# Performance work log

Hardware: AMD Instinct MI355X
Metric: run time of the kernel (lower is better)

The kernel has to match this reference:

```python
import jax, jax.numpy as jnp
from jax import lax
import numpy as np

EPS = 1e-5  # BatchNorm eps


def _gatv2(x, src, dst, Wl, Wr, att, bias, heads, d, concat):
    # x: [B, N, Fin]; src/dst: [E] (self-loops appended, PyG add_self_loops=True)
    B, N, _ = x.shape
    xl = jnp.einsum('bnf,of->bno', x, Wl).reshape(B, N, heads, d)  # source proj
    xr = jnp.einsum('bnf,of->bno', x, Wr).reshape(B, N, heads, d)  # target proj
    e = jax.nn.leaky_relu(xl[:, src] + xr[:, dst], 0.2)            # [B,E,H,d]
    logit = jnp.einsum('behd,hd->beh', e, att)                     # [B,E,H]
    seg_max = jax.vmap(lambda v: jax.ops.segment_max(v, dst, num_segments=N))
    seg_sum = jax.vmap(lambda v: jax.ops.segment_sum(v, dst, num_segments=N))
    m = seg_max(logit)                                             # [B,N,H]
    p = jnp.exp(logit - m[:, dst])
    alpha = p / seg_sum(p)[:, dst]                                 # edge softmax over targets
    out = seg_sum(alpha[..., None] * xl[:, src])                   # [B,N,H,d]
    out = out.reshape(B, N, heads * d) if concat else out.mean(2)
    return out + bias


def _bn(h, g, b, m, v):  # BatchNorm1d, eval mode (running stats)
    return (h - m) * (g / jnp.sqrt(v + EPS)) + b


def _lstm_layer(seq, Wih, Whh, bih, bhh):
    # seq: [BN, T, Hin]; gate order i,f,g,o (PyTorch)
    BN, T, _ = seq.shape
    H = Whh.shape[1]
    pre = jnp.einsum('bti,gi->tbg', seq, Wih) + bih + bhh          # [T,BN,4H]
    def step(carry, xp):
        h, c = carry
        g = xp + h @ Whh.T
        i, f, gg, o = jnp.split(g, 4, axis=-1)
        c = jax.nn.sigmoid(f) * c + jax.nn.sigmoid(i) * jnp.tanh(gg)
        h = jax.nn.sigmoid(o) * jnp.tanh(c)
        return (h, c), h
    h0 = jnp.zeros((BN, H), seq.dtype)
    _, hs = lax.scan(step, (h0, h0), pre)
    return jnp.swapaxes(hs, 0, 1)                                  # [BN,T,H]


def forward(x, edge_index, Wp, bp, Wl1, Wr1, a1, bg1, g1, be1, m1, v1,
            Wl2, Wr2, a2, bg2, g2, be2, m2, v2,
            Wih0, Whh0, bih0, bhh0, Wih1, Whh1, bih1, bhh1,
            Wa, ba, Ws1, bs1, Ws2, bs2, Wh1, bh1, Wh2, bh2):
    b, t, n, f = x.shape
    H = Wp.shape[0]
    loops = jnp.arange(n, dtype=edge_index.dtype)
    src = jnp.concatenate([edge_index[0], loops])
    dst = jnp.concatenate([edge_index[1], loops])
    xt = x.reshape(b * t, n, f)  # batch all (b,t) graph passes together
    h1 = jax.nn.elu(_bn(_gatv2(xt, src, dst, Wl1, Wr1, a1, bg1, 2, H, True), g1, be1, m1, v1))
    # dropout is identity in eval mode
    h2 = jax.nn.elu(_bn(_gatv2(h1, src, dst, Wl2, Wr2, a2, bg2, 1, H, False), g2, be2, m2, v2))
    h = h2 + jnp.einsum('bnf,hf->bnh', xt, Wp) + bp                # residual input_proj
    sp = h.reshape(b * n, t, H)  # replicates torch .view(b*n,t,H) on contiguous [b,t,n,H]
    lo = _lstm_layer(_lstm_layer(sp, Wih0, Whh0, bih0, bhh0), Wih1, Whh1, bih1, bhh1)
    aw = jax.nn.softmax(jnp.einsum('bth,oh->bto', lo, Wa) + ba, axis=1)
    ctx = (aw * lo).sum(1)                                         # [b*n, H]
    nb = Ws1.shape[1]
    sk = x[:, -1, :, :nb].reshape(b * n, nb)
    sk = jax.nn.gelu(sk @ Ws1.T + bs1, approximate=False) @ Ws2.T + bs2
    z = jnp.concatenate([ctx, sk], axis=1)
    z = jax.nn.gelu(z @ Wh1.T + bh1, approximate=False) @ Wh2.T + bh2
    return z.reshape(b, n, 1)


def setup_inputs() -> dict:
    key = jax.random.key(0)
    ks = jax.random.split(key, 40)
    b, t, n, f, H, E, nb = 4, 16, 1000, 32, 128, 16000, 13
    p = lambda k, s: (jax.random.normal(k, s) * 0.05).astype(jnp.float32)
    x = jax.random.normal(ks[0], (b, t, n, f), jnp.float32)
    src = jax.random.randint(ks[1], (E,), 0, n)
    dst = (src + jax.random.randint(ks[2], (E,), 1, n)) % n  # no accidental self-loops
    edge_index = jnp.stack([src, dst]).astype(jnp.int32)
    return dict(
        x=x, edge_index=edge_index,
        Wp=p(ks[3], (H, f)), bp=p(ks[4], (H,)),
        Wl1=p(ks[5], (2 * H, f)), Wr1=p(ks[6], (2 * H, f)), a1=p(ks[7], (2, H)), bg1=p(ks[8], (2 * H,)),
        g1=1.0 + p(ks[9], (2 * H,)), be1=p(ks[10], (2 * H,)), m1=p(ks[11], (2 * H,)),
        v1=jax.random.uniform(ks[12], (2 * H,), minval=0.5, maxval=1.5),
        Wl2=p(ks[13], (H, 2 * H)), Wr2=p(ks[14], (H, 2 * H)), a2=p(ks[15], (1, H)), bg2=p(ks[16], (H,)),
        g2=1.0 + p(ks[17], (H,)), be2=p(ks[18], (H,)), m2=p(ks[19], (H,)),
        v2=jax.random.uniform(ks[20], (H,), minval=0.5, maxval=1.5),
        Wih0=p(ks[21], (4 * H, H)), Whh0=p(ks[22], (4 * H, H)), bih0=p(ks[23], (4 * H,)), bhh0=p(ks[24], (4 * H,)),
        Wih1=p(ks[25], (4 * H, H)), Whh1=p(ks[26], (4 * H, H)), bih1=p(ks[27], (4 * H,)), bhh1=p(ks[28], (4 * H,)),
        Wa=p(ks[29], (1, H)), ba=p(ks[30], (1,)),
        Ws1=p(ks[31], (H // 2, nb)), bs1=p(ks[32], (H // 2,)),
        Ws2=p(ks[33], (H // 4, H // 2)), bs2=p(ks[34], (H // 4,)),
        Wh1=p(ks[35], (H // 2, H + H // 4)), bh1=p(ks[36], (H // 2,)),
        Wh2=p(ks[37], (1, H // 2)), bh2=p(ks[38], (1,)))


def reference(x, edge_index, Wp, bp, Wl1, Wr1, a1, bg1, g1, be1, m1, v1,
              Wl2, Wr2, a2, bg2, g2, be2, m2, v2,
              Wih0, Whh0, bih0, bhh0, Wih1, Whh1, bih1, bhh1,
              Wa, ba, Ws1, bs1, Ws2, bs2, Wh1, bh1, Wh2, bh2):
    return forward(x, edge_index, Wp, bp, Wl1, Wr1, a1, bg1, g1, be1, m1, v1,
                   Wl2, Wr2, a2, bg2, g2, be2, m2, v2,
                   Wih0, Whh0, bih0, bhh0, Wih1, Whh1, bih1, bhh1,
                   Wa, ba, Ws1, bs1, Ws2, bs2, Wh1, bh1, Wh2, bh2)
```

## Files before the change

kernel.cpp:

```cpp
#include <hip/hip_runtime.h>
#include <hip/hip_fp16.h>

#define EPS_BN 1e-5f

typedef __attribute__((ext_vector_type(8))) short bf16x8;
typedef __attribute__((ext_vector_type(4))) float f32x4;

#define O_SRCD   0u
#define O_DSTD   17024u
#define O_COUNTS 34048u
#define O_OFFS   35072u
#define O_CURS   36096u
#define O_EIDX   37120u
#define O_PW1    54144u
#define O_PW2    74624u
#define O_LW     140160u
#define O_BCOMB  402304u
#define O_ABF    403328u
#define O_HWT    404352u
#define O_BIG0   417536u
#define O_BIG1   (O_BIG0 + 16384000u)
#define O_BIG2   (O_BIG1 + 16384000u)
#define O_BIG3   (O_BIG2 + 16384000u)
#define O_BIG4   (O_BIG3 + 8192000u)
#define O_SXL    (O_BIG4 + 8192000u)

__device__ __forceinline__ float rsum32(float p) {
  p += __shfl_xor(p, 1);  p += __shfl_xor(p, 2);  p += __shfl_xor(p, 4);
  p += __shfl_xor(p, 8);  p += __shfl_xor(p, 16); return p;
}
__device__ __forceinline__ float rsum64(float p) {
  p = rsum32(p); p += __shfl_xor(p, 32); return p;
}
__device__ __forceinline__ float eluf(float x)  { return x > 0.f ? x : expm1f(x); }
__device__ __forceinline__ float geluf(float x) { return 0.5f * x * (1.f + erff(x * 0.70710678118654752f)); }
__device__ __forceinline__ unsigned short f2bf(float f) {
  unsigned int u = __float_as_uint(f);
  u += 0x7FFFu + ((u >> 16) & 1u);
  return (unsigned short)(u >> 16);
}
__device__ __forceinline__ float bf2f(unsigned short h) {
  return __uint_as_float(((unsigned int)h) << 16);
}
__device__ __forceinline__ unsigned short f2h(float x) {
  __half h = __float2half(x);
  return *reinterpret_cast<unsigned short*>(&h);
}
__device__ __forceinline__ float h2f(unsigned short u) {
  __half h = *reinterpret_cast<__half*>(&u);
  return __half2float(h);
}
__device__ __forceinline__ void unpk(unsigned int w, float& lo, float& hi) {
  lo = __uint_as_float(w << 16);
  hi = __uint_as_float(w & 0xFFFF0000u);
}

__global__ __launch_bounds__(1024)
void prep_all(const int* __restrict__ ei, int* __restrict__ srcD,
              int* __restrict__ dstD, int* __restrict__ offs,
              int* __restrict__ esrc)
{
  __shared__ int cnt[1024];
  __shared__ int cur[1000];
  const int tid = threadIdx.x;
  cnt[tid] = 0;
  __syncthreads();
  for (int i = tid; i < 17000; i += 1024) {
    int s = (i < 16000) ? ei[i] : (i - 16000);
    int d = (i < 16000) ? ei[16000 + i] : (i - 16000);
    srcD[i] = s; dstD[i] = d;
    atomicAdd(&cnt[d], 1);
  }
  __syncthreads();
  int v = cnt[tid];
  for (int d = 1; d < 1024; d <<= 1) {
    int t = (tid >= d) ? cnt[tid - d] : 0;
    __syncthreads();
    cnt[tid] += t;
    __syncthreads();
  }
  if (tid < 1000) { offs[tid + 1] = cnt[tid]; cur[tid] = cnt[tid] - v; }
  if (tid == 0) offs[0] = 0;
  __syncthreads();
  for (int i = tid; i < 17000; i += 1024) {
    int p = atomicAdd(&cur[dstD[i]], 1);
    esrc[p] = srcD[i];
  }
}

__global__ void pack_kernel(
    const float* __restrict__ Wl1, const float* __restrict__ Wr1, const float* __restrict__ Wp,
    const float* __restrict__ Wl2, const float* __restrict__ Wr2,
    const float* __restrict__ Wih0, const float* __restrict__ Whh0,
    const float* __restrict__ bih0, const float* __restrict__ bhh0,
    const float* __restrict__ Wih1, const float* __restrict__ Whh1,
    const float* __restrict__ bih1, const float* __restrict__ bhh1,
    const float* __restrict__ g1, const float* __restrict__ be1, const float* __restrict__ m1,
    const float* __restrict__ v1, const float* __restrict__ bg1,
    const float* __restrict__ g2, const float* __restrict__ be2, const float* __restrict__ m2,
    const float* __restrict__ v2, const float* __restrict__ bg2,
    const float* __restrict__ Ws1, const float* __restrict__ Ws2, const float* __restrict__ Wh1,
    const float* __restrict__ a1, const float* __restrict__ a2,
    float* __restrict__ PW1, unsigned short* __restrict__ PW2Bu,
    unsigned short* __restrict__ PHHBu, unsigned short* __restrict__ PWBu,
    float* __restrict__ BC, float* __restrict__ ABF, float* __restrict__ HWT,
    float* __restrict__ C1F, float* __restrict__ C2F)
{
  int i = blockIdx.x * 256 + threadIdx.x;
  if (i < 262144) {
    int e = i & 7, lane = (i >> 3) & 63, gt = (i >> 9) & 31,
        kc = (i >> 14) & 3, sp = (i >> 16) & 1, L = (i >> 17) & 1;
    int gp = (gt << 4) + (lane & 15);
    int jj = gp >> 2, gate = gp & 3;
    int kk = (kc << 5) + ((lane >> 4) << 3) + e;
    const float* Wih = L ? Wih1 : Wih0;
    const float* Whh = L ? Whh1 : Whh0;
    float wv = Wih[(gate * 128 + jj) * 128 + kk];
    unsigned short hi = f2bf(wv);
    PWBu[i] = (sp == 0) ? hi : f2bf(wv - bf2f(hi));
    float hv = Whh[(gate * 128 + jj) * 128 + kk];
    unsigned short hhi = f2bf(hv);
    PHHBu[i] = (sp == 0) ? hhi : f2bf(hv - bf2f(hhi));
  }
  if (i < 131072) {
    int e = i & 7, lane = (i >> 3) & 63, ct = (i >> 9) & 15,
        kc = (i >> 13) & 7, sp = (i >> 16) & 1;
    int c = (ct << 4) + (lane & 15);
    int k = (kc << 5) + ((lane >> 4) << 3) + e;
    float wv2 = (c < 128) ? Wl2[c * 256 + k] : Wr2[(c - 128) * 256 + k];
    unsigned short hi = f2bf(wv2);
    PW2Bu[i] = (sp == 0) ? hi : f2bf(wv2 - bf2f(hi));
  }
  if (i < 20480) { int g = i % 640, k = i / 640;
    PW1[i] = (g < 256) ? Wl1[g * 32 + k] : (g < 512) ? Wr1[(g - 256) * 32 + k]
                                                     : Wp[(g - 512) * 32 + k]; }
  if (i < 1024) { int u = i & 3, jj = (i >> 2) & 127, L = i >> 9;
    BC[i] = (L ? bih1 : bih0)[u * 128 + jj] + (L ? bhh1 : bhh0)[u * 128 + jj]; }
  if (i < 768) {
    if (i < 256) ABF[i] = g1[i] * rsqrtf(v1[i] + EPS_BN);
    else if (i < 512) { int c = i - 256; float a = g1[c] * rsqrtf(v1[c] + EPS_BN);
      ABF[i] = (bg1[c] - m1[c]) * a + be1[c]; }
    else if (i < 640) { int c = i - 512; ABF[i] = g2[c] * rsqrtf(v2[c] + EPS_BN); }
    else { int c = i - 640; float a = g2[c] * rsqrtf(v2[c] + EPS_BN);
      ABF[i] = (bg2[c] - m2[c]) * a + be2[c]; }
  }
  if (i < 13120) {
    if (i < 832) { int l = i & 63, c = i >> 6; HWT[i] = Ws1[l * 13 + c]; }
    else if (i < 2880) { int k = i - 832; int l = k & 31, jj = k >> 5; HWT[i] = Ws2[l * 64 + jj]; }
    else { int k = i - 2880; int l = k & 63, r = k >> 6; HWT[i] = Wh1[l * 160 + r]; }
  }
  if (i < 64) {
    int k = i & 31, h = i >> 5;
    float s = 0.f;
    for (int j = 0; j < 128; ++j)
      s = fmaf(a1[h * 128 + j], Wl1[(h * 128 + j) * 32 + k], s);
    C1F[i] = 0.6f * s;
  }
  if (i < 256) {
    float s = 0.f;
    for (int c = 0; c < 128; ++c)
      s = fmaf(a2[c], Wl2[c * 256 + i], s);
    C2F[i] = 0.6f * s;
  }
}

__global__ __launch_bounds__(320)
void proj1_kernel(const float* __restrict__ X, const float* __restrict__ PW1,
                  const float* __restrict__ bp, const float* __restrict__ C1F,
                  unsigned short* __restrict__ XL1u,
                  float* __restrict__ XR1, float* __restrict__ XP,
                  float* __restrict__ SXL1)
{
  __shared__ __align__(16) float xs[32][16];
  const int tid = threadIdx.x;
  const int r0 = blockIdx.x * 16;
  for (int el = tid; el < 512; el += 320) {
    int r = el >> 5, k = el & 31;
    xs[k][r] = X[(size_t)(r0 + r) * 32 + k];
  }
  __syncthreads();
  if (tid < 32) {
    int r = tid & 15, h = tid >> 4;
    const float* c1 = C1F + h * 32;
    float s = 0.f;
    for (int k = 0; k < 32; ++k) s = fmaf(c1[k], xs[k][r], s);
    SXL1[(size_t)(r0 + r) * 2 + h] = s;
  }
  const int gA = tid, gB = tid + 320;
  float accA[16], accB[16];
  const float iB = (gB >= 512) ? bp[gB - 512] : 0.f;
  #pragma unroll
  for (int r = 0; r < 16; ++r) { accA[r] = 0.f; accB[r] = iB; }
  for (int k = 0; k < 32; ++k) {
    float wA = PW1[k * 640 + gA], wB = PW1[k * 640 + gB];
    float xv[16];
    #pragma unroll
    for (int q = 0; q < 4; ++q)
      *reinterpret_cast<float4*>(&xv[q * 4]) = *reinterpret_cast<const float4*>(&xs[k][q * 4]);
    #pragma unroll
    for (int r = 0; r < 16; ++r) {
      accA[r] = fmaf(wA, xv[r], accA[r]);
      accB[r] = fmaf(wB, xv[r], accB[r]);
    }
  }
  for (int r = 0; r < 16; ++r) {
    size_t row = r0 + r;
    if (gA < 256) XL1u[row * 256 + gA] = f2bf(accA[r]);
    else          XR1[row * 256 + (gA - 256)] = accA[r];
    if (gB < 512) XR1[row * 256 + (gB - 256)] = accB[r];
    else          XP[row * 128 + (gB - 512)] = accB[r];
  }
}

__global__ __launch_bounds__(256)
void gat1_kernel(const unsigned short* __restrict__ XLu, const float* __restrict__ XR,
                 const float* __restrict__ SXL,
                 const int* __restrict__ esrc, const int* __restrict__ offs,
                 const float* __restrict__ a1, const float* __restrict__ ABF,
                 const float* __restrict__ C2F,
                 float* __restrict__ H1, float* __restrict__ SXL2)
{
  const int lane = threadIdx.x & 63;
  const int wv = threadIdx.x >> 6;
  const int n = blockIdx.x * 4 + wv;
  const int b = blockIdx.y;
  const int epar = lane >> 5;
  const int head = (lane >> 4) & 1;
  const int li = lane & 15;
  const int f0 = head * 128 + li * 8;
  const int beg = offs[n];
  const int deg = offs[n + 1] - beg;
  const uint4* XLb = reinterpret_cast<const uint4*>(XLu) + (size_t)b * 32000 + (f0 >> 3);
  const float* SXLb = SXL + (size_t)b * 2000;
  float xr[8], av[8];
  {
    const float* xrp = XR + (size_t)(b * 1000 + n) * 256 + f0;
    float4 t0 = *reinterpret_cast<const float4*>(xrp);
    float4 t1 = *reinterpret_cast<const float4*>(xrp + 4);
    xr[0]=t0.x; xr[1]=t0.y; xr[2]=t0.z; xr[3]=t0.w;
    xr[4]=t1.x; xr[5]=t1.y; xr[6]=t1.z; xr[7]=t1.w;
    const float* ap = a1 + f0;
    float4 a0 = *reinterpret_cast<const float4*>(ap);
    float4 a1v = *reinterpret_cast<const float4*>(ap + 4);
    av[0]=a0.x; av[1]=a0.y; av[2]=a0.z; av[3]=a0.w;
    av[4]=a1v.x; av[5]=a1v.y; av[6]=a1v.z; av[7]=a1v.w;
  }
  float ssum = 0.f, acc[8];
  #pragma unroll
  for (int k = 0; k < 8; ++k) acc[k] = 0.f;
  bool v = epar < deg;
  int sC = esrc[beg + (v ? epar : 0)];
  uint4 u = XLb[(size_t)sC * 32];
  float slxC = SXLb[sC * 2 + head];
  for (int i0 = 0; i0 < deg; i0 += 2) {
    int nmy = i0 + 2 + epar;
    bool nv = nmy < deg;
    int sN = esrc[beg + (nv ? nmy : 0)];
    uint4 un = XLb[(size_t)sN * 32];
    float slxN = SXLb[sN * 2 + head];
    float x[8];
    unpk(u.x, x[0], x[1]); unpk(u.y, x[2], x[3]);
    unpk(u.z, x[4], x[5]); unpk(u.w, x[6], x[7]);
    float p = 0.f;
    #pragma unroll
    for (int k = 0; k < 8; ++k)
      p = fmaf(av[k], fabsf(x[k] + xr[k]), p);
    p += __shfl_xor(p, 1); p += __shfl_xor(p, 2);
    p += __shfl_xor(p, 4); p += __shfl_xor(p, 8);
    float we = v ? __expf(fmaf(0.4f, p, slxC)) : 0.f;
    ssum += we;
    #pragma unroll
    for (int k = 0; k < 8; ++k) acc[k] = fmaf(we, x[k], acc[k]);
    v = nv; u = un; slxC = slxN;
  }
  ssum += __shfl_xor(ssum, 32);
  float inv = 1.f / ssum;
  float A4[8], B4[8];
  {
    const float* aap = ABF + f0;
    float4 t0 = *reinterpret_cast<const float4*>(aap);
    float4 t1 = *reinterpret_cast<const float4*>(aap + 4);
    A4[0]=t0.x; A4[1]=t0.y; A4[2]=t0.z; A4[3]=t0.w;
    A4[4]=t1.x; A4[5]=t1.y; A4[6]=t1.z; A4[7]=t1.w;
    const float* bbp = ABF + 256 + f0;
    float4 s0v = *reinterpret_cast<const float4*>(bbp);
    float4 s1v = *reinterpret_cast<const float4*>(bbp + 4);
    B4[0]=s0v.x; B4[1]=s0v.y; B4[2]=s0v.z; B4[3]=s0v.w;
    B4[4]=s1v.x; B4[5]=s1v.y; B4[6]=s1v.z; B4[7]=s1v.w;
  }
  float o[8];
  #pragma unroll
  for (int k = 0; k < 8; ++k) {
    float A = acc[k] + __shfl_xor(acc[k], 32);
    o[k] = eluf(fmaf(A * inv, A4[k], B4[k]));
  }
  {
    const float* cp = C2F + f0;
    float4 c0 = *reinterpret_cast<const float4*>(cp);
    float4 c1 = *reinterpret_cast<const float4*>(cp + 4);
    float cc[8] = {c0.x, c0.y, c0.z, c0.w, c1.x, c1.y, c1.z, c1.w};
    float s2 = 0.f;
    #pragma unroll
    for (int k = 0; k < 8; ++k) s2 = fmaf(cc[k], o[k], s2);
    s2 += __shfl_xor(s2, 1); s2 += __shfl_xor(s2, 2);
    s2 += __shfl_xor(s2, 4); s2 += __shfl_xor(s2, 8);
    s2 += __shfl_xor(s2, 16);
    if (lane == 0) SXL2[(size_t)b * 1000 + n] = s2;
  }
  if (lane < 32) {
    float* hp = H1 + (size_t)(b * 1000 + n) * 256 + f0;
    *reinterpret_cast<float4*>(hp) = make_float4(o[0], o[1], o[2], o[3]);
    *reinterpret_cast<float4*>(hp + 4) = make_float4(o[4], o[5], o[6], o[7]);
  }
}

__global__ __launch_bounds__(512)
void proj2_kernel(const float* __restrict__ H1, const unsigned short* __restrict__ PW2B,
                  unsigned short* __restrict__ XL2u, float* __restrict__ XR2)
{
  const int tid = threadIdx.x;
  const int lane = tid & 63;
  const int wv = tid >> 6;
  const int l15 = lane & 15;
  const int kg = lane >> 4;
  const int r0 = blockIdx.x * 32;
  f32x4 acc[2][2];
  #pragma unroll
  for (int rt = 0; rt < 2; ++rt)
    #pragma unroll
    for (int ct = 0; ct < 2; ++ct)
      #pragma unroll
      for (int e = 0; e < 4; ++e) acc[rt][ct][e] = 0.f;
  for (int kc = 0; kc < 8; ++kc) {
    bf16x8 xh[2], xl[2];
    #pragma unroll
    for (int rt = 0; rt < 2; ++rt) {
      const float* xp = H1 + (size_t)(r0 + rt * 16 + l15) * 256 + (kc << 5) + (kg << 3);
      float4 va = *reinterpret_cast<const float4*>(xp);
      float4 vb = *reinterpret_cast<const float4*>(xp + 4);
      float xs[8] = {va.x, va.y, va.z, va.w, vb.x, vb.y, vb.z, vb.w};
      #pragma unroll
      for (int e = 0; e < 8; ++e) {
        unsigned short h = f2bf(xs[e]);
        xh[rt][e] = (short)h;
        xl[rt][e] = (short)f2bf(xs[e] - bf2f(h));
      }
    }
    #pragma unroll
    for (int ct = 0; ct < 2; ++ct) {
      const int ctg = (wv << 1) + ct;
      const unsigned short* wp = PW2B + ((size_t)(kc * 16 + ctg)) * 512 + lane * 8;
      bf16x8 whi = *reinterpret_cast<const bf16x8*>(wp);
      bf16x8 wlo = *reinterpret_cast<const bf16x8*>(wp + 65536);
      #pragma unroll
      for (int rt = 0; rt < 2; ++rt) {
        acc[rt][ct] = __builtin_amdgcn_mfma_f32_16x16x32_bf16(xh[rt], whi, acc[rt][ct], 0, 0, 0);
        acc[rt][ct] = __builtin_amdgcn_mfma_f32_16x16x32_bf16(xh[rt], wlo, acc[rt][ct], 0, 0, 0);
        acc[rt][ct] = __builtin_amdgcn_mfma_f32_16x16x32_bf16(xl[rt], whi, acc[rt][ct], 0, 0, 0);
      }
    }
  }
  #pragma unroll
  for (int ct = 0; ct < 2; ++ct) {
    const int col = (wv << 5) + (ct << 4) + l15;
    #pragma unroll
    for (int rt = 0; rt < 2; ++rt) {
      #pragma unroll
      for (int reg = 0; reg < 4; ++reg) {
        const int row = r0 + rt * 16 + (kg << 2) + reg;
        float val = acc[rt][ct][reg];
        if (col < 128) XL2u[(size_t)row * 128 + col] = f2bf(val);
        else           XR2[(size_t)row * 128 + (col - 128)] = val;
      }
    }
  }
}

__global__ __launch_bounds__(256)
void gat2_kernel(const unsigned short* __restrict__ XLu, const float* __restrict__ XR,
                 const float* __restrict__ SXL,
                 const int* __restrict__ esrc, const int* __restrict__ offs,
                 const float* __restrict__ a2, const float* __restrict__ ABF,
                 const float* __restrict__ XP, float* __restrict__ Hout)
{
  const int lane = threadIdx.x & 63;
  const int wv = threadIdx.x >> 6;
  const int n = blockIdx.x * 4 + wv;
  const int b = blockIdx.y;
  const int grp = lane >> 4;
  const int li = lane & 15;
  const int f0 = li * 8;
  const int beg = offs[n];
  const int deg = offs[n + 1] - beg;
  const uint4* XLb = reinterpret_cast<const uint4*>(XLu) + (size_t)b * 16000 + li;
  const float* SXLb = SXL + (size_t)b * 1000;
  float xr[8], av[8];
  {
    const float* xrp = XR + (size_t)(b * 1000 + n) * 128 + f0;
    float4 t0 = *reinterpret_cast<const float4*>(xrp);
    float4 t1 = *reinterpret_cast<const float4*>(xrp + 4);
    xr[0]=t0.x; xr[1]=t0.y; xr[2]=t0.z; xr[3]=t0.w;
    xr[4]=t1.x; xr[5]=t1.y; xr[6]=t1.z; xr[7]=t1.w;
    const float* ap = a2 + f0;
    float4 a0 = *reinterpret_cast<const float4*>(ap);
    float4 a1v = *reinterpret_cast<const float4*>(ap + 4);
    av[0]=a0.x; av[1]=a0.y; av[2]=a0.z; av[3]=a0.w;
    av[4]=a1v.x; av[5]=a1v.y; av[6]=a1v.z; av[7]=a1v.w;
  }
  float ssum = 0.f, acc[8];
  #pragma unroll
  for (int k = 0; k < 8; ++k) acc[k] = 0.f;
  bool v = grp < deg;
  int sC = esrc[beg + (v ? grp : 0)];
  uint4 u = XLb[(size_t)sC * 16];
  float slxC = SXLb[sC];
  for (int i0 = 0; i0 < deg; i0 += 4) {
    int nmy = i0 + 4 + grp;
    bool nv = nmy < deg;
    int sN = esrc[beg + (nv ? nmy : 0)];
    uint4 un = XLb[(size_t)sN * 16];
    float slxN = SXLb[sN];
    float x[8];
    unpk(u.x, x[0], x[1]); unpk(u.y, x[2], x[3]);
    unpk(u.z, x[4], x[5]); unpk(u.w, x[6], x[7]);
    float p = 0.f;
    #pragma unroll
    for (int k = 0; k < 8; ++k)
      p = fmaf(av[k], fabsf(x[k] + xr[k]), p);
    p += __shfl_xor(p, 1); p += __shfl_xor(p, 2);
    p += __shfl_xor(p, 4); p += __shfl_xor(p, 8);
    float we = v ? __expf(fmaf(0.4f, p, slxC)) : 0.f;
    ssum += we;
    #pragma unroll
    for (int k = 0; k < 8; ++k) acc[k] = fmaf(we, x[k], acc[k]);
    v = nv; u = un; slxC = slxN;
  }
  ssum += __shfl_xor(ssum, 16);
  ssum += __shfl_xor(ssum, 32);
  #pragma unroll
  for (int k = 0; k < 8; ++k) {
    acc[k] += __shfl_xor(acc[k], 16);
    acc[k] += __shfl_xor(acc[k], 32);
  }
  float inv = 1.f / ssum;
  if (lane < 16) {
    const float* aap = ABF + 512 + f0;
    float4 t0 = *reinterpret_cast<const float4*>(aap);
    float4 t1 = *reinterpret_cast<const float4*>(aap + 4);
    const float* bbp = ABF + 640 + f0;
    float4 s0v = *reinterpret_cast<const float4*>(bbp);
    float4 s1v = *reinterpret_cast<const float4*>(bbp + 4);
    const float* xpp = XP + (size_t)(b * 1000 + n) * 128 + f0;
    float4 p0 = *reinterpret_cast<const float4*>(xpp);
    float4 p1 = *reinterpret_cast<const float4*>(xpp + 4);
    float A4[8] = {t0.x, t0.y, t0.z, t0.w, t1.x, t1.y, t1.z, t1.w};
    float B4[8] = {s0v.x, s0v.y, s0v.z, s0v.w, s1v.x, s1v.y, s1v.z, s1v.w};
    float P4[8] = {p0.x, p0.y, p0.z, p0.w, p1.x, p1.y, p1.z, p1.w};
    float o[8];
    #pragma unroll
    for (int k = 0; k < 8; ++k)
      o[k] = eluf(fmaf(acc[k] * inv, A4[k], B4[k])) + P4[k];
    float* hp = Hout + (size_t)(b * 1000 + n) * 128 + f0;
    *reinterpret_cast<float4*>(hp) = make_float4(o[0], o[1], o[2], o[3]);
    *reinterpret_cast<float4*>(hp + 4) = make_float4(o[4], o[5], o[6], o[7]);
  }
}

__global__ __launch_bounds__(512)
void gemm_pre_kernel(const float* __restrict__ X, const unsigned short* __restrict__ PWB,
                     const float* __restrict__ BCL, unsigned short* __restrict__ PREh)
{
  const int tid = threadIdx.x;
  const int lane = tid & 63;
  const int wv = tid >> 6;
  const int l15 = lane & 15;
  const int kg = lane >> 4;
  const int r0 = blockIdx.x * 32;
  f32x4 acc[2][4];
  #pragma unroll
  for (int rt = 0; rt < 2; ++rt)
    #pragma unroll
    for (int gt = 0; gt < 4; ++gt)
      #pragma unroll
      for (int e = 0; e < 4; ++e) acc[rt][gt][e] = 0.f;
  for (int kc = 0; kc < 4; ++kc) {
    bf16x8 xh[2], xl[2];
    #pragma unroll
    for (int rt = 0; rt < 2; ++rt) {
      const float* xp = X + (size_t)(r0 + rt * 16 + l15) * 128 + (kc << 5) + (kg << 3);
      float4 va = *reinterpret_cast<const float4*>(xp);
      float4 vb = *reinterpret_cast<const float4*>(xp + 4);
      float xs[8] = {va.x, va.y, va.z, va.w, vb.x, vb.y, vb.z, vb.w};
      #pragma unroll
      for (int e = 0; e < 8; ++e) {
        unsigned short h = f2bf(xs[e]);
        xh[rt][e] = (short)h;
        xl[rt][e] = (short)f2bf(xs[e] - bf2f(h));
      }
    }
    #pragma unroll
    for (int gt = 0; gt < 4; ++gt) {
      const int gtg = (wv << 2) + gt;
      const unsigned short* wp = PWB + ((size_t)(kc * 32 + gtg)) * 512 + lane * 8;
      bf16x8 whi = *reinterpret_cast<const bf16x8*>(wp);
      bf16x8 wlo = *reinterpret_cast<const bf16x8*>(wp + 65536);
      #pragma unroll
      for (int rt = 0; rt < 2; ++rt) {
        acc[rt][gt] = __builtin_amdgcn_mfma_f32_16x16x32_bf16(xh[rt], whi, acc[rt][gt], 0, 0, 0);
        acc[rt][gt] = __builtin_amdgcn_mfma_f32_16x16x32_bf16(xh[rt], wlo, acc[rt][gt], 0, 0, 0);
        acc[rt][gt] = __builtin_amdgcn_mfma_f32_16x16x32_bf16(xl[rt], whi, acc[rt][gt], 0, 0, 0);
      }
    }
  }
  #pragma unroll
  for (int gt = 0; gt < 4; ++gt) {
    const int col = (wv << 6) + (gt << 4) + l15;
    const float bias = BCL[col];
    #pragma unroll
    for (int rt = 0; rt < 2; ++rt) {
      #pragma unroll
      for (int reg = 0; reg < 4; ++reg) {
        const int row = r0 + rt * 16 + (kg << 2) + reg;
        PREh[(size_t)row * 512 + col] = f2h(acc[rt][gt][reg] + bias);
      }
    }
  }
}

__device__ __forceinline__ float cellf(float4 g, float& c) {
  const float ig = 1.f / (1.f + __expf(-g.x));
  const float fg = 1.f / (1.f + __expf(-g.y));
  const float gg = tanhf(g.z);
  const float og = 1.f / (1.f + __expf(-g.w));
  c = fmaf(fg, c, ig * gg);
  return og * tanhf(c);
}

__global__ __launch_bounds__(512)
void rec2_kernel(const unsigned short* __restrict__ PREh,
                 const unsigned short* __restrict__ PHHB,
                 float* __restrict__ HOUT)
{
  __shared__ unsigned short whi[65536];
  __shared__ unsigned short afr[2][4][64][8];
  const int tid = threadIdx.x;
  const int lane = tid & 63;
  const int w = tid >> 6;
  const int l15 = lane & 15;
  const int kg = lane >> 4;
  const int q0 = blockIdx.x << 4;
  for (int i = tid; i < 8192; i += 512)
    reinterpret_cast<uint4*>(whi)[i] = reinterpret_cast<const uint4*>(PHHB)[i];
  reinterpret_cast<uint4*>(&afr[0][0][0][0])[tid] = make_uint4(0u, 0u, 0u, 0u);
  const unsigned short* wloG = PHHB + 65536;
  float cs[4] = {0.f, 0.f, 0.f, 0.f};
  const int qq = l15 & 3;
  const int uu = l15 >> 2;
  const int seq = (kg << 2) + qq;
  for (int t = 0; t < 16; ++t) {
    __syncthreads();
    bf16x8 ah[4], al[4];
    #pragma unroll
    for (int kc = 0; kc < 4; ++kc) {
      ah[kc] = *reinterpret_cast<const bf16x8*>(&afr[0][kc][lane][0]);
      al[kc] = *reinterpret_cast<const bf16x8*>(&afr[1][kc][lane][0]);
    }
    f32x4 acc[4];
    #pragma unroll
    for (int gl = 0; gl < 4; ++gl)
      #pragma unroll
      for (int e = 0; e < 4; ++e) acc[gl][e] = 0.f;
    #pragma unroll
    for (int gl = 0; gl < 4; ++gl) {
      const int gt = (w << 2) + gl;
      #pragma unroll
      for (int kc = 0; kc < 4; ++kc) {
        const int off = ((kc * 32 + gt) * 64 + lane) * 8;
        bf16x8 wh = *reinterpret_cast<const bf16x8*>(&whi[off]);
        bf16x8 wl = *reinterpret_cast<const bf16x8*>(&wloG[off]);
        acc[gl] = __builtin_amdgcn_mfma_f32_16x16x32_bf16(ah[kc], wh, acc[gl], 0, 0, 0);
        acc[gl] = __builtin_amdgcn_mfma_f32_16x16x32_bf16(ah[kc], wl, acc[gl], 0, 0, 0);
        acc[gl] = __builtin_amdgcn_mfma_f32_16x16x32_bf16(al[kc], wh, acc[gl], 0, 0, 0);
      }
    }
    __syncthreads();
    const int row = ((q0 + seq) << 4) + t;
    #pragma unroll
    for (int gl = 0; gl < 4; ++gl) {
      const int gt = (w << 2) + gl;
      float in0 = acc[gl][0], in1 = acc[gl][1], in2 = acc[gl][2], in3 = acc[gl][3];
      float s0 = __shfl_xor(in1, 1), s1 = __shfl_xor(in0, 1),
            s2 = __shfl_xor(in3, 1), s3 = __shfl_xor(in2, 1);
      const bool b0 = (qq & 1);
      float t0 = b0 ? s0 : in0;
      float t1 = b0 ? in1 : s1;
      float t2 = b0 ? s2 : in2;
      float t3 = b0 ? in3 : s3;
      float u0 = __shfl_xor(t2, 2), u1 = __shfl_xor(t3, 2),
            u2 = __shfl_xor(t0, 2), u3 = __shfl_xor(t1, 2);
      const bool b1 = (qq & 2);
      float g0 = b1 ? u0 : t0;
      float g1 = b1 ? u1 : t1;
      float g2 = b1 ? t2 : u2;
      float g3 = b1 ? t3 : u3;
      const unsigned short* pp = PREh + (size_t)row * 512 + (gt << 4) + (uu << 2);
      ushort4 pu = *reinterpret_cast<const ushort4*>(pp);
      float4 gv = make_float4(g0 + h2f(pu.x), g1 + h2f(pu.y),
                              g2 + h2f(pu.z), g3 + h2f(pu.w));
      float h = cellf(gv, cs[gl]);
      const int unit = (gt << 2) + uu;
      HOUT[(size_t)row * 128 + unit] = h;
      if (t < 15) {
        unsigned short hh = f2bf(h);
        unsigned short hl = f2bf(h - bf2f(hh));
        const int kc2 = unit >> 5;
        const int lane2 = seq | (((unit & 31) >> 3) << 4);
        const int e2 = unit & 7;
        afr[0][kc2][lane2][e2] = hh;
        afr[1][kc2][lane2][e2] = hl;
      }
    }
  }
}

__global__ __launch_bounds__(64)
void attn_kernel(const float* __restrict__ LO, const float* __restrict__ X,
                 const float* __restrict__ Wa, const float* __restrict__ ba,
                 const float* __restrict__ bs1, const float* __restrict__ bs2,
                 const float* __restrict__ bh1, const float* __restrict__ bh2,
                 const float* __restrict__ Wh2, const float* __restrict__ HWT,
                 float* __restrict__ out)
{
  const int q = blockIdx.x, l = threadIdx.x;
  const float* lob = LO + (size_t)q * 2048;
  float loa[16], lobv[16];
  #pragma unroll
  for (int t = 0; t < 16; ++t) {
    loa[t]  = lob[t * 128 + l];
    lobv[t] = lob[t * 128 + 64 + l];
  }
  const float wa = Wa[l], wb = Wa[64 + l];
  float sc[16];
  #pragma unroll
  for (int t = 0; t < 16; ++t) sc[t] = rsum64(loa[t] * wa + lobv[t] * wb) + ba[0];
  float mx = sc[0];
  #pragma unroll
  for (int t = 1; t < 16; ++t) mx = fmaxf(mx, sc[t]);
  float den = 0.f;
  #pragma unroll
  for (int t = 0; t < 16; ++t) { sc[t] = __expf(sc[t] - mx); den += sc[t]; }
  const float inv = 1.f / den;
  float ca = 0.f, cb = 0.f;
  #pragma unroll
  for (int t = 0; t < 16; ++t) {
    float wgt = sc[t] * inv;
    ca = fmaf(wgt, loa[t], ca);
    cb = fmaf(wgt, lobv[t], cb);
  }
  __shared__ float zsh[160];
  __shared__ float hsk[64];
  __shared__ float skin[16];
  zsh[l] = ca; zsh[64 + l] = cb;
  const int bb = q / 1000, nn = q - bb * 1000;
  if (l < 13) skin[l] = X[(size_t)((bb * 16 + 15) * 1000 + nn) * 32 + l];
  __syncthreads();
  float h1 = bs1[l];
  for (int c = 0; c < 13; ++c) h1 = fmaf(skin[c], HWT[c * 64 + l], h1);
  h1 = geluf(h1);
  hsk[l] = h1;
  __syncthreads();
  if (l < 32) {
    float a = bs2[l];
    for (int jj = 0; jj < 64; ++jj) a = fmaf(hsk[jj], HWT[832 + jj * 32 + l], a);
    zsh[128 + l] = a;
  }
  __syncthreads();
  float hh = bh1[l];
  for (int r = 0; r < 160; ++r) hh = fmaf(zsh[r], HWT[2880 + r * 64 + l], hh);
  hh = geluf(hh);
  float s = rsum64(hh * Wh2[l]);
  if (l == 0) out[q] = s + bh2[0];
}

extern "C" void kernel_launch(void* const* d_in, const int* in_sizes, int n_in,
                              void* d_out, int out_size, void* d_ws, size_t ws_size,
                              hipStream_t stream)
{
  const float* x    = (const float*)d_in[0];
  const int*   ei   = (const int*)d_in[1];
  const float* Wp   = (const float*)d_in[2];
  const float* bp   = (const float*)d_in[3];
  const float* Wl1  = (const float*)d_in[4];
  const float* Wr1  = (const float*)d_in[5];
  const float* a1   = (const float*)d_in[6];
  const float* bg1  = (const float*)d_in[7];
  const float* g1   = (const float*)d_in[8];
  const float* be1  = (const float*)d_in[9];
  const float* m1   = (const float*)d_in[10];
  const float* v1   = (const float*)d_in[11];
  const float* Wl2  = (const float*)d_in[12];
  const float* Wr2  = (const float*)d_in[13];
  const float* a2   = (const float*)d_in[14];
  const float* bg2  = (const float*)d_in[15];
  const float* g2   = (const float*)d_in[16];
  const float* be2  = (const float*)d_in[17];
  const float* m2   = (const float*)d_in[18];
  const float* v2   = (const float*)d_in[19];
  const float* Wih0 = (const float*)d_in[20];
  const float* Whh0 = (const float*)d_in[21];
  const float* bih0 = (const float*)d_in[22];
  const float* bhh0 = (const float*)d_in[23];
  const float* Wih1 = (const float*)d_in[24];
  const float* Whh1 = (const float*)d_in[25];
  const float* bih1 = (const float*)d_in[26];
  const float* bhh1 = (const float*)d_in[27];
  const float* Wa   = (const float*)d_in[28];
  const float* ba   = (const float*)d_in[29];
  const float* Ws1  = (const float*)d_in[30];
  const float* bs1  = (const float*)d_in[31];
  const float* Ws2  = (const float*)d_in[32];
  const float* bs2  = (const float*)d_in[33];
  const float* Wh1  = (const float*)d_in[34];
  const float* bh1  = (const float*)d_in[35];
  const float* Wh2  = (const float*)d_in[36];
  const float* bh2  = (const float*)d_in[37];

  float* ws = (float*)d_ws;
  int* srcD   = (int*)(ws + O_SRCD);
  int* dstD   = (int*)(ws + O_DSTD);
  int* offs   = (int*)(ws + O_OFFS);
  int* esrc   = (int*)(ws + O_EIDX);
  float* PW1  = ws + O_PW1;
  unsigned short* PW2Bu = (unsigned short*)(ws + O_PW2);
  unsigned short* PHHBu = (unsigned short*)(ws + O_LW);
  unsigned short* PWBu  = (unsigned short*)(ws + O_LW + 131072u);
  float* BC   = ws + O_BCOMB;
  float* ABF  = ws + O_ABF;
  float* HWT  = ws + O_HWT;
  unsigned short* XL1u = (unsigned short*)(ws + O_BIG0);
  float* XR1  = ws + O_BIG1;
  float* H1   = ws + O_BIG2;
  float* XP   = ws + O_BIG3;
  float* Hres = ws + O_BIG4;
  unsigned short* XL2u = (unsigned short*)(ws + O_BIG0);
  float* XR2  = ws + O_BIG0 + 8192000u;
  unsigned short* PREh = (unsigned short*)(ws + O_BIG0);
  float* H1SEQ = ws + O_BIG2;
  float* LOp  = ws + O_BIG3;
  float* SXL1 = ws + O_SXL;
  float* SXL2 = ws + O_SXL + 128000u;
  float* C1F  = ws + O_SXL + 192000u;
  float* C2F  = ws + O_SXL + 192064u;
  float* outp = (float*)d_out;

  prep_all<<<1, 1024, 0, stream>>>(ei, srcD, dstD, offs, esrc);
  pack_kernel<<<1024, 256, 0, stream>>>(Wl1, Wr1, Wp, Wl2, Wr2,
      Wih0, Whh0, bih0, bhh0, Wih1, Whh1, bih1, bhh1,
      g1, be1, m1, v1, bg1, g2, be2, m2, v2, bg2,
      Ws1, Ws2, Wh1, a1, a2, PW1, PW2Bu, PHHBu, PWBu, BC, ABF, HWT, C1F, C2F);
  proj1_kernel<<<4000, 320, 0, stream>>>(x, PW1, bp, C1F, XL1u, XR1, XP, SXL1);
  gat1_kernel<<<dim3(250, 64), 256, 0, stream>>>(XL1u, XR1, SXL1, esrc, offs, a1, ABF,
                                                 C2F, H1, SXL2);
  proj2_kernel<<<2000, 512, 0, stream>>>(H1, PW2Bu, XL2u, XR2);
  gat2_kernel<<<dim3(250, 64), 256, 0, stream>>>(XL2u, XR2, SXL2, esrc, offs, a2, ABF, XP, Hres);
  gemm_pre_kernel<<<2000, 512, 0, stream>>>(Hres, PWBu, BC, PREh);
  rec2_kernel<<<250, 512, 0, stream>>>(PREh, PHHBu, H1SEQ);
  gemm_pre_kernel<<<2000, 512, 0, stream>>>(H1SEQ, PWBu + 131072u, BC + 512, PREh);
  rec2_kernel<<<250, 512, 0, stream>>>(PREh, PHHBu + 131072u, LOp);
  attn_kernel<<<4000, 64, 0, stream>>>(LOp, x, Wa, ba, bs1, bs2, bh1, bh2, Wh2, HWT, outp);
}
```

Before: 560.0 us.

## Store intermediate activations as bf16 and drop split-precision MFMA passes

All large intermediate tensors (XR1, XP, H1, XR2, Hres, LSTM hidden outputs) are now written and read as bf16 instead of fp32, roughly halving global memory traffic between kernels. The GEMMs for proj2 and the LSTM input projection now load bf16 activations directly and skip the hi/lo activation split, going from three MFMAs per tile to two. The single-block edge CSR build is also split into four multi-block kernels. The cost is lower precision in the activations passed between stages and three extra kernel launches.

Result: faster. 477.9 us (-14.7%).

```diff
diff --git a/kernel.cpp b/kernel.cpp
--- a/kernel.cpp
+++ b/kernel.cpp
@@ -54,38 +54,45 @@
   lo = __uint_as_float(w << 16);
   hi = __uint_as_float(w & 0xFFFF0000u);
 }
-
-__global__ __launch_bounds__(1024)
-void prep_all(const int* __restrict__ ei, int* __restrict__ srcD,
-              int* __restrict__ dstD, int* __restrict__ offs,
-              int* __restrict__ esrc)
-{
-  __shared__ int cnt[1024];
-  __shared__ int cur[1000];
-  const int tid = threadIdx.x;
-  cnt[tid] = 0;
-  __syncthreads();
-  for (int i = tid; i < 17000; i += 1024) {
+__device__ __forceinline__ void unpk8(uint4 u, float (&x)[8]) {
+  unpk(u.x, x[0], x[1]); unpk(u.y, x[2], x[3]);
+  unpk(u.z, x[4], x[5]); unpk(u.w, x[6], x[7]);
+}
+
+__global__ void prep_edges(const int* __restrict__ ei, int* __restrict__ srcD,
+                           int* __restrict__ dstD, int* __restrict__ counts) {
+  int i = blockIdx.x * 256 + threadIdx.x;
+  if (i < 1024) counts[i] = 0;
+  if (i < 17000) {
     int s = (i < 16000) ? ei[i] : (i - 16000);
     int d = (i < 16000) ? ei[16000 + i] : (i - 16000);
     srcD[i] = s; dstD[i] = d;
-    atomicAdd(&cnt[d], 1);
-  }
+  }
+}
+__global__ void hist_kernel(const int* __restrict__ dstD, int* __restrict__ counts) {
+  int i = blockIdx.x * 256 + threadIdx.x;
+  if (i < 17000) atomicAdd(&counts[dstD[i]], 1);
+}
+__global__ void scan_kernel(const int* __restrict__ counts, int* __restrict__ offs,
+                            int* __restrict__ curs) {
+  __shared__ int sh[1024];
+  int i = threadIdx.x;
+  int v = (i < 1000) ? counts[i] : 0;
+  sh[i] = v;
   __syncthreads();
-  int v = cnt[tid];
   for (int d = 1; d < 1024; d <<= 1) {
-    int t = (tid >= d) ? cnt[tid - d] : 0;
+    int t = (i >= d) ? sh[i - d] : 0;
     __syncthreads();
-    cnt[tid] += t;
+    sh[i] += t;
     __syncthreads();
   }
-  if (tid < 1000) { offs[tid + 1] = cnt[tid]; cur[tid] = cnt[tid] - v; }
-  if (tid == 0) offs[0] = 0;
-  __syncthreads();
-  for (int i = tid; i < 17000; i += 1024) {
-    int p = atomicAdd(&cur[dstD[i]], 1);
-    esrc[p] = srcD[i];
-  }
+  if (i < 1000) { offs[i + 1] = sh[i]; curs[i] = sh[i] - v; }
+  if (i == 0) offs[0] = 0;
+}
+__global__ void fill_kernel(const int* __restrict__ srcD, const int* __restrict__ dstD,
+                            int* __restrict__ curs, int* __restrict__ esrc) {
+  int i = blockIdx.x * 256 + threadIdx.x;
+  if (i < 17000) { int p = atomicAdd(&curs[dstD[i]], 1); esrc[p] = srcD[i]; }
 }
 
 __global__ void pack_kernel(
@@ -168,7 +175,7 @@
 void proj1_kernel(const float* __restrict__ X, const float* __restrict__ PW1,
                   const float* __restrict__ bp, const float* __restrict__ C1F,
                   unsigned short* __restrict__ XL1u,
-                  float* __restrict__ XR1, float* __restrict__ XP,
+                  unsigned short* __restrict__ XR1u, unsigned short* __restrict__ XPu,
                   float* __restrict__ SXL1)
 {
   __shared__ __align__(16) float xs[32][16];
@@ -206,19 +213,19 @@
   for (int r = 0; r < 16; ++r) {
     size_t row = r0 + r;
     if (gA < 256) XL1u[row * 256 + gA] = f2bf(accA[r]);
-    else          XR1[row * 256 + (gA - 256)] = accA[r];
-    if (gB < 512) XR1[row * 256 + (gB - 256)] = accB[r];
-    else          XP[row * 128 + (gB - 512)] = accB[r];
+    else          XR1u[row * 256 + (gA - 256)] = f2bf(accA[r]);
+    if (gB < 512) XR1u[row * 256 + (gB - 256)] = f2bf(accB[r]);
+    else          XPu[row * 128 + (gB - 512)] = f2bf(accB[r]);
   }
 }
 
 __global__ __launch_bounds__(256)
-void gat1_kernel(const unsigned short* __restrict__ XLu, const float* __restrict__ XR,
+void gat1_kernel(const unsigned short* __restrict__ XLu, const unsigned short* __restrict__ XRu,
                  const float* __restrict__ SXL,
                  const int* __restrict__ esrc, const int* __restrict__ offs,
                  const float* __restrict__ a1, const float* __restrict__ ABF,
                  const float* __restrict__ C2F,
-                 float* __restrict__ H1, float* __restrict__ SXL2)
+                 unsigned short* __restrict__ H1u, float* __restrict__ SXL2)
 {
   const int lane = threadIdx.x & 63;
   const int wv = threadIdx.x >> 6;
@@ -234,11 +241,8 @@
   const float* SXLb = SXL + (size_t)b * 2000;
   float xr[8], av[8];
   {
-    const float* xrp = XR + (size_t)(b * 1000 + n) * 256 + f0;
-    float4 t0 = *reinterpret_cast<const float4*>(xrp);
-    float4 t1 = *reinterpret_cast<const float4*>(xrp + 4);
-    xr[0]=t0.x; xr[1]=t0.y; xr[2]=t0.z; xr[3]=t0.w;
-    xr[4]=t1.x; xr[5]=t1.y; xr[6]=t1.z; xr[7]=t1.w;
+    const uint4* xrp = reinterpret_cast<const uint4*>(XRu + (size_t)(b * 1000 + n) * 256 + f0);
+    unpk8(xrp[0], xr);
     const float* ap = a1 + f0;
     float4 a0 = *reinterpret_cast<const float4*>(ap);
     float4 a1v = *reinterpret_cast<const float4*>(ap + 4);
@@ -259,8 +263,7 @@
     uint4 un = XLb[(size_t)sN * 32];
     float slxN = SXLb[sN * 2 + head];
     float x[8];
-    unpk(u.x, x[0], x[1]); unpk(u.y, x[2], x[3]);
-    unpk(u.z, x[4], x[5]); unpk(u.w, x[6], x[7]);
+    unpk8(u, x);
     float p = 0.f;
     #pragma unroll
     for (int k = 0; k < 8; ++k)
@@ -308,15 +311,17 @@
     if (lane == 0) SXL2[(size_t)b * 1000 + n] = s2;
   }
   if (lane < 32) {
-    float* hp = H1 + (size_t)(b * 1000 + n) * 256 + f0;
-    *reinterpret_cast<float4*>(hp) = make_float4(o[0], o[1], o[2], o[3]);
-    *reinterpret_cast<float4*>(hp + 4) = make_float4(o[4], o[5], o[6], o[7]);
+    unsigned short* hp = H1u + (size_t)(b * 1000 + n) * 256 + f0;
+    ushort4 w0 = make_ushort4(f2bf(o[0]), f2bf(o[1]), f2bf(o[2]), f2bf(o[3]));
+    ushort4 w1 = make_ushort4(f2bf(o[4]), f2bf(o[5]), f2bf(o[6]), f2bf(o[7]));
+    *reinterpret_cast<ushort4*>(hp) = w0;
+    *reinterpret_cast<ushort4*>(hp + 4) = w1;
   }
 }
 
 __global__ __launch_bounds__(512)
-void proj2_kernel(const float* __restrict__ H1, const unsigned short* __restrict__ PW2B,
-                  unsigned short* __restrict__ XL2u, float* __restrict__ XR2)
+void proj2_kernel(const unsigned short* __restrict__ H1u, const unsigned short* __restrict__ PW2B,
+                  unsigned short* __restrict__ XL2u, unsigned short* __restrict__ XR2u)
 {
   const int tid = threadIdx.x;
   const int lane = tid & 63;
@@ -332,20 +337,11 @@
       #pragma unroll
       for (int e = 0; e < 4; ++e) acc[rt][ct][e] = 0.f;
   for (int kc = 0; kc < 8; ++kc) {
-    bf16x8 xh[2], xl[2];
-    #pragma unroll
-    for (int rt = 0; rt < 2; ++rt) {
-      const float* xp = H1 + (size_t)(r0 + rt * 16 + l15) * 256 + (kc << 5) + (kg << 3);
-      float4 va = *reinterpret_cast<const float4*>(xp);
-      float4 vb = *reinterpret_cast<const float4*>(xp + 4);
-      float xs[8] = {va.x, va.y, va.z, va.w, vb.x, vb.y, vb.z, vb.w};
-      #pragma unroll
-      for (int e = 0; e < 8; ++e) {
-        unsigned short h = f2bf(xs[e]);
-        xh[rt][e] = (short)h;
-        xl[rt][e] = (short)f2bf(xs[e] - bf2f(h));
-      }
-    }
+    bf16x8 xa[2];
+    #pragma unroll
+    for (int rt = 0; rt < 2; ++rt)
+      xa[rt] = *reinterpret_cast<const bf16x8*>(
+          H1u + (size_t)(r0 + rt * 16 + l15) * 256 + (kc << 5) + (kg << 3));
     #pragma unroll
     for (int ct = 0; ct < 2; ++ct) {
       const int ctg = (wv << 1) + ct;
@@ -354,9 +350,8 @@
       bf16x8 wlo = *reinterpret_cast<const bf16x8*>(wp + 65536);
       #pragma unroll
       for (int rt = 0; rt < 2; ++rt) {
-        acc[rt][ct] = __builtin_amdgcn_mfma_f32_16x16x32_bf16(xh[rt], whi, acc[rt][ct], 0, 0, 0);
-        acc[rt][ct] = __builtin_amdgcn_mfma_f32_16x16x32_bf16(xh[rt], wlo, acc[rt][ct], 0, 0, 0);
-        acc[rt][ct] = __builtin_amdgcn_mfma_f32_16x16x32_bf16(xl[rt], whi, acc[rt][ct], 0, 0, 0);
+        acc[rt][ct] = __builtin_amdgcn_mfma_f32_16x16x32_bf16(xa[rt], whi, acc[rt][ct], 0, 0, 0);
+        acc[rt][ct] = __builtin_amdgcn_mfma_f32_16x16x32_bf16(xa[rt], wlo, acc[rt][ct], 0, 0, 0);
       }
     }
   }
@@ -368,20 +363,20 @@
       #pragma unroll
       for (int reg = 0; reg < 4; ++reg) {
         const int row = r0 + rt * 16 + (kg << 2) + reg;
-        float val = acc[rt][ct][reg];
-        if (col < 128) XL2u[(size_t)row * 128 + col] = f2bf(val);
-        else           XR2[(size_t)row * 128 + (col - 128)] = val;
+        unsigned short val = f2bf(acc[rt][ct][reg]);
+        if (col < 128) XL2u[(size_t)row * 128 + col] = val;
+        else           XR2u[(size_t)row * 128 + (col - 128)] = val;
       }
     }
   }
 }
 
 __global__ __launch_bounds__(256)
-void gat2_kernel(const unsigned short* __restrict__ XLu, const float* __restrict__ XR,
+void gat2_kernel(const unsigned short* __restrict__ XLu, const unsigned short* __restrict__ XRu,
                  const float* __restrict__ SXL,
                  const int* __restrict__ esrc, const int* __restrict__ offs,
                  const float* __restrict__ a2, const float* __restrict__ ABF,
-                 const float* __restrict__ XP, float* __restrict__ Hout)
+                 const unsigned short* __restrict__ XPu, unsigned short* __restrict__ Hresu)
 {
   const int lane = threadIdx.x & 63;
   const int wv = threadIdx.x >> 6;
@@ -396,11 +391,8 @@
   const float* SXLb = SXL + (size_t)b * 1000;
   float xr[8], av[8];
   {
-    const float* xrp = XR + (size_t)(b * 1000 + n) * 128 + f0;
-    float4 t0 = *reinterpret_cast<const float4*>(xrp);
-    float4 t1 = *reinterpret_cast<const float4*>(xrp + 4);
-    xr[0]=t0.x; xr[1]=t0.y; xr[2]=t0.z; xr[3]=t0.w;
-    xr[4]=t1.x; xr[5]=t1.y; xr[6]=t1.z; xr[7]=t1.w;
+    const uint4* xrp = reinterpret_cast<const uint4*>(XRu + (size_t)(b * 1000 + n) * 128 + f0);
+    unpk8(xrp[0], xr);
     const float* ap = a2 + f0;
     float4 a0 = *reinterpret_cast<const float4*>(ap);
     float4 a1v = *reinterpret_cast<const float4*>(ap + 4);
@@ -421,8 +413,7 @@
     uint4 un = XLb[(size_t)sN * 16];
     float slxN = SXLb[sN];
     float x[8];
-    unpk(u.x, x[0], x[1]); unpk(u.y, x[2], x[3]);
-    unpk(u.z, x[4], x[5]); unpk(u.w, x[6], x[7]);
+    unpk8(u, x);
     float p = 0.f;
     #pragma unroll
     for (int k = 0; k < 8; ++k)
@@ -450,24 +441,27 @@
     const float* bbp = ABF + 640 + f0;
     float4 s0v = *reinterpret_cast<const float4*>(bbp);
     float4 s1v = *reinterpret_cast<const float4*>(bbp + 4);
-    const float* xpp = XP + (size_t)(b * 1000 + n) * 128 + f0;
-    float4 p0 = *reinterpret_cast<const float4*>(xpp);
-    float4 p1 = *reinterpret_cast<const float4*>(xpp + 4);
+    float xp8[8];
+    unpk8(*reinterpret_cast<const uint4*>(XPu + (size_t)(b * 1000 + n) * 128 + f0), xp8);
     float A4[8] = {t0.x, t0.y, t0.z, t0.w, t1.x, t1.y, t1.z, t1.w};
     float B4[8] = {s0v.x, s0v.y, s0v.z, s0v.w, s1v.x, s1v.y, s1v.z, s1v.w};
-    float P4[8] = {p0.x, p0.y, p0.z, p0.w, p1.x, p1.y, p1.z, p1.w};
-    float o[8];
-    #pragma unroll
-    for (int k = 0; k < 8; ++k)
-      o[k] = eluf(fmaf(acc[k] * inv, A4[k], B4[k])) + P4[k];
-    float* hp = Hout + (size_t)(b * 1000 + n) * 128 + f0;
-    *reinterpret_cast<float4*>(hp) = make_float4(o[0], o[1], o[2], o[3]);
-    *reinterpret_cast<float4*>(hp + 4) = make_float4(o[4], o[5], o[6], o[7]);
+    unsigned short* hp = Hresu + (size_t)(b * 1000 + n) * 128 + f0;
+    ushort4 w0, w1;
+    w0.x = f2bf(eluf(fmaf(acc[0] * inv, A4[0], B4[0])) + xp8[0]);
+    w0.y = f2bf(eluf(fmaf(acc[1] * inv, A4[1], B4[1])) + xp8[1]);
+    w0.z = f2bf(eluf(fmaf(acc[2] * inv, A4[2], B4[2])) + xp8[2]);
+    w0.w = f2bf(eluf(fmaf(acc[3] * inv, A4[3], B4[3])) + xp8[3]);
+    w1.x = f2bf(eluf(fmaf(acc[4] * inv, A4[4], B4[4])) + xp8[4]);
+    w1.y = f2bf(eluf(fmaf(acc[5] * inv, A4[5], B4[5])) + xp8[5]);
+    w1.z = f2bf(eluf(fmaf(acc[6] * inv, A4[6], B4[6])) + xp8[6]);
+    w1.w = f2bf(eluf(fmaf(acc[7] * inv, A4[7], B4[7])) + xp8[7]);
+    *reinterpret_cast<ushort4*>(hp) = w0;
+    *reinterpret_cast<ushort4*>(hp + 4) = w1;
   }
 }
 
 __global__ __launch_bounds__(512)
-void gemm_pre_kernel(const float* __restrict__ X, const unsigned short* __restrict__ PWB,
+void gemm_pre_kernel(const unsigned short* __restrict__ Xu, const unsigned short* __restrict__ PWB,
                      const float* __restrict__ BCL, unsigned short* __restrict__ PREh)
 {
   const int tid = threadIdx.x;
@@ -484,20 +478,11 @@
       #pragma unroll
       for (int e = 0; e < 4; ++e) acc[rt][gt][e] = 0.f;
   for (int kc = 0; kc < 4; ++kc) {
-    bf16x8 xh[2], xl[2];
-    #pragma unroll
-    for (int rt = 0; rt < 2; ++rt) {
-      const float* xp = X + (size_t)(r0 + rt * 16 + l15) * 128 + (kc << 5) + (kg << 3);
-      float4 va = *reinterpret_cast<const float4*>(xp);
-      float4 vb = *reinterpret_cast<const float4*>(xp + 4);
-      float xs[8] = {va.x, va.y, va.z, va.w, vb.x, vb.y, vb.z, vb.w};
-      #pragma unroll
-      for (int e = 0; e < 8; ++e) {
-        unsigned short h = f2bf(xs[e]);
-        xh[rt][e] = (short)h;
-        xl[rt][e] = (short)f2bf(xs[e] - bf2f(h));
-      }
-    }
+    bf16x8 xa[2];
+    #pragma unroll
+    for (int rt = 0; rt < 2; ++rt)
+      xa[rt] = *reinterpret_cast<const bf16x8*>(
+          Xu + (size_t)(r0 + rt * 16 + l15) * 128 + (kc << 5) + (kg << 3));
     #pragma unroll
     for (int gt = 0; gt < 4; ++gt) {
       const int gtg = (wv << 2) + gt;
@@ -506,9 +491,8 @@
       bf16x8 wlo = *reinterpret_cast<const bf16x8*>(wp + 65536);
       #pragma unroll
       for (int rt = 0; rt < 2; ++rt) {
-        acc[rt][gt] = __builtin_amdgcn_mfma_f32_16x16x32_bf16(xh[rt], whi, acc[rt][gt], 0, 0, 0);
-        acc[rt][gt] = __builtin_amdgcn_mfma_f32_16x16x32_bf16(xh[rt], wlo, acc[rt][gt], 0, 0, 0);
-        acc[rt][gt] = __builtin_amdgcn_mfma_f32_16x16x32_bf16(xl[rt], whi, acc[rt][gt], 0, 0, 0);
+        acc[rt][gt] = __builtin_amdgcn_mfma_f32_16x16x32_bf16(xa[rt], whi, acc[rt][gt], 0, 0, 0);
+        acc[rt][gt] = __builtin_amdgcn_mfma_f32_16x16x32_bf16(xa[rt], wlo, acc[rt][gt], 0, 0, 0);
       }
     }
   }
@@ -539,7 +523,7 @@
 __global__ __launch_bounds__(512)
 void rec2_kernel(const unsigned short* __restrict__ PREh,
                  const unsigned short* __restrict__ PHHB,
-                 float* __restrict__ HOUT)
+                 unsigned short* __restrict__ HOUTu)
 {
   __shared__ unsigned short whi[65536];
   __shared__ unsigned short afr[2][4][64][8];
@@ -609,9 +593,9 @@
                               g2 + h2f(pu.z), g3 + h2f(pu.w));
       float h = cellf(gv, cs[gl]);
       const int unit = (gt << 2) + uu;
-      HOUT[(size_t)row * 128 + unit] = h;
+      unsigned short hh = f2bf(h);
+      HOUTu[(size_t)row * 128 + unit] = hh;
       if (t < 15) {
-        unsigned short hh = f2bf(h);
         unsigned short hl = f2bf(h - bf2f(hh));
         const int kc2 = unit >> 5;
         const int lane2 = seq | (((unit & 31) >> 3) << 4);
@@ -624,7 +608,7 @@
 }
 
 __global__ __launch_bounds__(64)
-void attn_kernel(const float* __restrict__ LO, const float* __restrict__ X,
+void attn_kernel(const unsigned short* __restrict__ LOu, const float* __restrict__ X,
                  const float* __restrict__ Wa, const float* __restrict__ ba,
                  const float* __restrict__ bs1, const float* __restrict__ bs2,
                  const float* __restrict__ bh1, const float* __restrict__ bh2,
@@ -632,12 +616,12 @@
                  float* __restrict__ out)
 {
   const int q = blockIdx.x, l = threadIdx.x;
-  const float* lob = LO + (size_t)q * 2048;
+  const unsigned short* lob = LOu + (size_t)q * 2048;
   float loa[16], lobv[16];
   #pragma unroll
   for (int t = 0; t < 16; ++t) {
-    loa[t]  = lob[t * 128 + l];
-    lobv[t] = lob[t * 128 + 64 + l];
+    loa[t]  = bf2f(lob[t * 128 + l]);
+    lobv[t] = bf2f(lob[t * 128 + 64 + l]);
   }
   const float wa = Wa[l], wb = Wa[64 + l];
   float sc[16];
@@ -728,7 +712,9 @@
   float* ws = (float*)d_ws;
   int* srcD   = (int*)(ws + O_SRCD);
   int* dstD   = (int*)(ws + O_DSTD);
+  int* counts = (int*)(ws + O_COUNTS);
   int* offs   = (int*)(ws + O_OFFS);
+  int* curs   = (int*)(ws + O_CURS);
   int* esrc   = (int*)(ws + O_EIDX);
   float* PW1  = ws + O_PW1;
   unsigned short* PW2Bu = (unsigned short*)(ws + O_PW2);
@@ -738,34 +724,38 @@
   float* ABF  = ws + O_ABF;
   float* HWT  = ws + O_HWT;
   unsigned short* XL1u = (unsigned short*)(ws + O_BIG0);
-  float* XR1  = ws + O_BIG1;
-  float* H1   = ws + O_BIG2;
-  float* XP   = ws + O_BIG3;
-  float* Hres = ws + O_BIG4;
+  unsigned short* XR1u = (unsigned short*)(ws + O_BIG1);
+  unsigned short* H1u  = (unsigned short*)(ws + O_BIG2);
+  unsigned short* XPu  = (unsigned short*)(ws + O_BIG3);
+  unsigned short* Hresu = (unsigned short*)(ws + O_BIG4);
   unsigned short* XL2u = (unsigned short*)(ws + O_BIG0);
-  float* XR2  = ws + O_BIG0 + 8192000u;
+  unsigned short* XR2u = (unsigned short*)(ws + O_BIG0 + 8192000u);
   unsigned short* PREh = (unsigned short*)(ws + O_BIG0);
-  float* H1SEQ = ws + O_BIG2;
-  float* LOp  = ws + O_BIG3;
+  unsigned short* H1SEQu = (unsigned short*)(ws + O_BIG2);
+  unsigned short* LOu  = (unsigned short*)(ws + O_BIG3);
   float* SXL1 = ws + O_SXL;
   float* SXL2 = ws + O_SXL + 128000u;
   float* C1F  = ws + O_SXL + 192000u;
   float* C2F  = ws + O_SXL + 192064u;
   float* outp = (float*)d_out;
 
-  prep_all<<<1, 1024, 0, stream>>>(ei, srcD, dstD, offs, esrc);
+  prep_edges<<<67, 256, 0, stream>>>(ei, srcD, dstD, counts);
+  hist_kernel<<<67, 256, 0, stream>>>(dstD, counts);
+  scan_kernel<<<1, 1024, 0, stream>>>(counts, offs, curs);
+  fill_kernel<<<67, 256, 0, stream>>>(srcD, dstD, curs, esrc);
   pack_kernel<<<1024, 256, 0, stream>>>(Wl1, Wr1, Wp, Wl2, Wr2,
       Wih0, Whh0, bih0, bhh0, Wih1, Whh1, bih1, bhh1,
       g1, be1, m1, v1, bg1, g2, be2, m2, v2, bg2,
       Ws1, Ws2, Wh1, a1, a2, PW1, PW2Bu, PHHBu, PWBu, BC, ABF, HWT, C1F, C2F);
-  proj1_kernel<<<4000, 320, 0, stream>>>(x, PW1, bp, C1F, XL1u, XR1, XP, SXL1);
-  gat1_kernel<<<dim3(250, 64), 256, 0, stream>>>(XL1u, XR1, SXL1, esrc, offs, a1, ABF,
-                                                 C2F, H1, SXL2);
-  proj2_kernel<<<2000, 512, 0, stream>>>(H1, PW2Bu, XL2u, XR2);
-  gat2_kernel<<<dim3(250, 64), 256, 0, stream>>>(XL2u, XR2, SXL2, esrc, offs, a2, ABF, XP, Hres);
-  gemm_pre_kernel<<<2000, 512, 0, stream>>>(Hres, PWBu, BC, PREh);
-  rec2_kernel<<<250, 512, 0, stream>>>(PREh, PHHBu, H1SEQ);
-  gemm_pre_kernel<<<2000, 512, 0, stream>>>(H1SEQ, PWBu + 131072u, BC + 512, PREh);
-  rec2_kernel<<<250, 512, 0, stream>>>(PREh, PHHBu + 131072u, LOp);
-  attn_kernel<<<4000, 64, 0, stream>>>(LOp, x, Wa, ba, bs1, bs2, bh1, bh2, Wh2, HWT, outp);
-}
+  proj1_kernel<<<4000, 320, 0, stream>>>(x, PW1, bp, C1F, XL1u, XR1u, XPu, SXL1);
+  gat1_kernel<<<dim3(250, 64), 256, 0, stream>>>(XL1u, XR1u, SXL1, esrc, offs, a1, ABF,
+                                                 C2F, H1u, SXL2);
+  proj2_kernel<<<2000, 512, 0, stream>>>(H1u, PW2Bu, XL2u, XR2u);
+  gat2_kernel<<<dim3(250, 64), 256, 0, stream>>>(XL2u, XR2u, SXL2, esrc, offs, a2, ABF,
+                                                 XPu, Hresu);
+  gemm_pre_kernel<<<2000, 512, 0, stream>>>(Hresu, PWBu, BC, PREh);
+  rec2_kernel<<<250, 512, 0, stream>>>(PREh, PHHBu, H1SEQu);
+  gemm_pre_kernel<<<2000, 512, 0, stream>>>(H1SEQu, PWBu + 131072u, BC + 512, PREh);
+  rec2_kernel<<<250, 512, 0, stream>>>(PREh, PHHBu + 131072u, LOu);
+  attn_kernel<<<4000, 64, 0, stream>>>(LOu, x, Wa, ba, bs1, bs2, bh1, bh2, Wh2, HWT, outp);
+}
```
